# Performance work log

Hardware: AMD Instinct MI355X
Metric: run time of the kernel (lower is better)

The kernel has to match this reference:

```python
import jax, jax.numpy as jnp
import numpy as np

B, NPG, D_IN, D, L = 64, 512, 1, 128, 10
N = B * NPG
DEG = 16
E = N * DEG
EPS = 1e-5


def setup_inputs() -> dict:
    key = jax.random.key(0)
    ks = jax.random.split(key, 8)
    x = jax.random.normal(ks[0], (N, D_IN), jnp.float32)
    # edges confined within each graph: local indices + per-graph offset
    src_local = jax.random.randint(ks[1], (E,), 0, NPG)
    dst_local = jax.random.randint(ks[2], (E,), 0, NPG)
    offs = (jnp.arange(E) // (E // B)) * NPG
    edge_src = (src_local + offs).astype(jnp.int32)
    edge_dst = (dst_local + offs).astype(jnp.int32)
    batch = jnp.repeat(jnp.arange(B, dtype=jnp.int32), NPG)
    g = lambda k, s, fan: jax.random.normal(k, s, jnp.float32) / np.float32(np.sqrt(fan))
    W0 = g(ks[3], (D_IN, D), D_IN)
    b0 = jnp.zeros((D,), jnp.float32)
    W_rest = g(ks[4], (L - 1, D, D), D)
    b_rest = jnp.zeros((L - 1, D), jnp.float32)
    gamma = jnp.ones((L, D), jnp.float32)
    beta = jnp.zeros((L, D), jnp.float32)
    W_att = g(ks[5], (D, D), D)
    return dict(x=x, edge_src=edge_src, edge_dst=edge_dst, batch=batch,
                W0=W0, b0=b0, W_rest=W_rest, b_rest=b_rest,
                gamma=gamma, beta=beta, W_att=W_att)


def _gcn_conv(h, W, b, src, dst, norm_e, self_w):
    # GCNConv: h' = D^-1/2 (A + I) D^-1/2 (h W) + b  (symmetric norm, self-loops)
    h = h @ W
    msg = norm_e[:, None] * h[src]                      # [E, D] gather
    agg = jax.ops.segment_sum(msg, dst, num_segments=N)  # [N, D] scatter-add
    return agg + self_w[:, None] * h + b


def _bn_relu(h, g, b):
    mu = jnp.mean(h, axis=0)
    var = jnp.var(h, axis=0)
    return jax.nn.relu(g * (h - mu) * jax.lax.rsqrt(var + EPS) + b)


def reference(x, edge_src, edge_dst, batch, W0, b0, W_rest, b_rest, gamma, beta, W_att):
    # symmetric GCN normalization with self-loops (edge weight 1)
    deg = 1.0 + jax.ops.segment_sum(jnp.ones((E,), x.dtype), edge_dst, num_segments=N)
    dinv = jax.lax.rsqrt(deg)
    norm_e = dinv[edge_src] * dinv[edge_dst]   # [E]
    self_w = dinv * dinv                        # [N] self-loop coefficient

    h = _gcn_conv(x, W0, b0, edge_src, edge_dst, norm_e, self_w)
    h = _bn_relu(h, gamma[0], beta[0])
    for l in range(L - 1):
        h = _gcn_conv(h, W_rest[l], b_rest[l], edge_src, edge_dst, norm_e, self_w)
        h = _bn_relu(h, gamma[l + 1], beta[l + 1])

    # graph attention pooling
    mean = jax.ops.segment_sum(h, batch, num_segments=B) / jnp.float32(NPG)  # [B, D]
    tg = jnp.tanh(mean @ W_att)                                              # [B, D]
    coefs = jax.nn.sigmoid(jnp.sum(h * tg[batch], axis=1) * 10.0)            # [N]
    graph_feat = jax.ops.segment_sum(coefs[:, None] * h, batch, num_segments=B)  # [B, D]

    # to_dense_batch (equal-sized graphs -> exact reshape) + concat broadcast graph feat
    node_dense = h.reshape(B, NPG, D)
    gf = jnp.broadcast_to(graph_feat[:, None, :], (B, NPG, D))
    return jnp.concatenate([node_dense, gf], axis=-1)  # [B, NPG, 2D]
```

## Files before the change

kernel.cpp:

```cpp
#include <hip/hip_runtime.h>
#include <hip/hip_bf16.h>
#include <math.h>

#define NN 32768
#define BG 64
#define NPGC 512
#define DD 128
#define EE 524288
#define LL 10
#define EPSF 1e-5f
#define PADK 72
#define PADW 136

typedef __attribute__((ext_vector_type(8))) short short8;
typedef __attribute__((ext_vector_type(4))) float float4v;

static __device__ __forceinline__ unsigned short f2bf(float x) {
    __hip_bfloat16 b = __float2bfloat16(x);
    return *reinterpret_cast<unsigned short*>(&b);
}
static __device__ __forceinline__ float bf2f(unsigned short u) {
    unsigned int v = ((unsigned int)u) << 16;
    return __uint_as_float(v);
}
static __device__ __forceinline__ void splitbf(float x, unsigned short& h, unsigned short& l) {
    unsigned short hh = f2bf(x);
    h = hh;
    l = f2bf(x - bf2f(hh));
}


__global__ void k_histM(const int* __restrict__ src, const int* __restrict__ dst,
                        unsigned int* __restrict__ Mp, int* __restrict__ cnt) {
    int e = blockIdx.x * 256 + threadIdx.x;
    int d = dst[e], s = src[e] & 511;
    int cell = (d << 9) + s;
    atomicAdd(&Mp[cell >> 1], 1u << ((cell & 1) << 4));
    atomicAdd(&cnt[d], 1);
}

__global__ void k_dinv(const int* __restrict__ cnt, float* __restrict__ dinv) {
    int n = blockIdx.x * 256 + threadIdx.x;
    dinv[n] = rsqrtf(1.0f + (float)cnt[n]);
}

__global__ void k_conv(const unsigned int* __restrict__ Mp, unsigned short* __restrict__ Mh) {
    int idx = (blockIdx.x * 256 + threadIdx.x) * 8;
    uint4 v = *(const uint4*)(Mp + (idx >> 1));
    unsigned int c[8] = {v.x & 0xffffu, v.x >> 16, v.y & 0xffffu, v.y >> 16,
                         v.z & 0xffffu, v.z >> 16, v.w & 0xffffu, v.w >> 16};
    int diag = (idx >> 9) & 511;
    int cb = idx & 511;
    unsigned short us[8];
    #pragma unroll
    for (int j = 0; j < 8; j++)
        us[j] = f2bf((float)(c[j] + ((cb + j == diag) ? 1u : 0u)));
    *(uint4*)(Mh + idx) = *(uint4*)us;
}

__global__ void k_wt(const float* __restrict__ Wr, unsigned short* __restrict__ Wt_h,
                     unsigned short* __restrict__ Wt_l) {
    int idx = blockIdx.x * 256 + threadIdx.x;
    int l = idx >> 14, rem = idx & 16383;
    int fp = rem >> 7, f = rem & 127;
    unsigned short h, lo;
    splitbf(Wr[l * 16384 + f * 128 + fp], h, lo);
    Wt_h[idx] = h;
    Wt_l[idx] = lo;
}

__global__ void k_l0(const float* __restrict__ x, const float* __restrict__ W0,
                     const float* __restrict__ dinv,
                     unsigned short* __restrict__ hwT_h, unsigned short* __restrict__ hwT_l) {
    int u = blockIdx.x * 256 + threadIdx.x;
    int f = u >> 12, n0 = (u & 4095) * 8;
    float w = W0[f];
    float4 xa = *(const float4*)(x + n0);
    float4 xb = *(const float4*)(x + n0 + 4);
    float4 da = *(const float4*)(dinv + n0);
    float4 db = *(const float4*)(dinv + n0 + 4);
    float v[8] = {xa.x * w * da.x, xa.y * w * da.y, xa.z * w * da.z, xa.w * w * da.w,
                  xb.x * w * db.x, xb.y * w * db.y, xb.z * w * db.z, xb.w * w * db.w};
    unsigned short uh[8], ul[8];
    #pragma unroll
    for (int i = 0; i < 8; i++) splitbf(v[i], uh[i], ul[i]);
    *(uint4*)(hwT_h + (size_t)f * NN + n0) = *(uint4*)uh;
    *(uint4*)(hwT_l + (size_t)f * NN + n0) = *(uint4*)ul;
}

__global__ __launch_bounds__(256) void k_aggmm(const unsigned short* __restrict__ Mh,
        const unsigned short* __restrict__ hwT_h, const unsigned short* __restrict__ hwT_l,
        const float* __restrict__ dinv, const float* __restrict__ bias,
        float* __restrict__ pre, float* __restrict__ stats) {
    __shared__ unsigned short As[64 * PADK];
    __shared__ unsigned short Bs_h[128 * PADK], Bs_l[128 * PADK];
    int t = threadIdx.x, lane = t & 63, wv = t >> 6;
    int l15 = lane & 15, quad = lane >> 4;
    int b = blockIdx.x, r = b & 7, q = b >> 3;
    int g = r + 8 * (q & 7);
    int mb = (q >> 3) * 64;
    size_t arow = ((size_t)g * 512 + mb) * 512;
    size_t gcol = (size_t)g * 512;
    float4v acc[8];
    #pragma unroll
    for (int i = 0; i < 8; i++) acc[i] = (float4v)0.f;

    for (int kc = 0; kc < 512; kc += 64) {
        __syncthreads();
        {
            int i = t >> 7;
            #pragma unroll
            for (int it = 0; it < 2; it++) {
                int u = t + it * 256;
                int row = u >> 3, ko = (u & 7) * 8;
                *(uint4*)(&As[row * PADK + ko]) =
                    *(const uint4*)(Mh + arow + (size_t)row * 512 + kc + ko);
            }
            (void)i;
        }
        #pragma unroll
        for (int i = 0; i < 4; i++) {
            int u = t + i * 256;
            int f = u >> 3, ko = (u & 7) * 8;
            size_t go = (size_t)f * NN + gcol + kc + ko;
            *(uint4*)(&Bs_h[f * PADK + ko]) = *(const uint4*)(hwT_h + go);
            *(uint4*)(&Bs_l[f * PADK + ko]) = *(const uint4*)(hwT_l + go);
        }
        __syncthreads();
        int f0 = wv * 32;
        #pragma unroll
        for (int ks = 0; ks < 2; ks++) {
            int kb = ks * 32 + quad * 8;
            short8 a[4];
            #pragma unroll
            for (int mt = 0; mt < 4; mt++)
                a[mt] = *(const short8*)(&As[(mt * 16 + l15) * PADK + kb]);
            #pragma unroll
            for (int nt = 0; nt < 2; nt++) {
                short8 bh = *(const short8*)(&Bs_h[(f0 + nt * 16 + l15) * PADK + kb]);
                short8 bl = *(const short8*)(&Bs_l[(f0 + nt * 16 + l15) * PADK + kb]);
                #pragma unroll
                for (int mt = 0; mt < 4; mt++) {
                    acc[mt * 2 + nt] = __builtin_amdgcn_mfma_f32_16x16x32_bf16(a[mt], bh, acc[mt * 2 + nt], 0, 0, 0);
                    acc[mt * 2 + nt] = __builtin_amdgcn_mfma_f32_16x16x32_bf16(a[mt], bl, acc[mt * 2 + nt], 0, 0, 0);
                }
            }
        }
    }
    int gbase = g * 512 + mb;
    int fA = wv * 32 + l15;
    float bf0 = bias[fA], bf1 = bias[fA + 16];
    float cs[2] = {0.f, 0.f}, cq[2] = {0.f, 0.f};
    #pragma unroll
    for (int mt = 0; mt < 4; mt++) {
        int n0 = gbase + mt * 16 + quad * 4;
        float4 dv = *(const float4*)(dinv + n0);
        #pragma unroll
        for (int nt = 0; nt < 2; nt++) {
            int f = fA + nt * 16;
            float bf = nt ? bf1 : bf0;
            float4v a = acc[mt * 2 + nt];
            float v0 = fmaf(dv.x, a[0], bf);
            float v1 = fmaf(dv.y, a[1], bf);
            float v2 = fmaf(dv.z, a[2], bf);
            float v3 = fmaf(dv.w, a[3], bf);
            pre[(size_t)(n0 + 0) * 128 + f] = v0;
            pre[(size_t)(n0 + 1) * 128 + f] = v1;
            pre[(size_t)(n0 + 2) * 128 + f] = v2;
            pre[(size_t)(n0 + 3) * 128 + f] = v3;
            cs[nt] += v0 + v1 + v2 + v3;
            cq[nt] = fmaf(v0, v0, cq[nt]); cq[nt] = fmaf(v1, v1, cq[nt]);
            cq[nt] = fmaf(v2, v2, cq[nt]); cq[nt] = fmaf(v3, v3, cq[nt]);
        }
    }
    #pragma unroll
    for (int nt = 0; nt < 2; nt++) {
        float cs_ = cs[nt], cq_ = cq[nt];
        cs_ += __shfl_xor(cs_, 16); cs_ += __shfl_xor(cs_, 32);
        cq_ += __shfl_xor(cq_, 16); cq_ += __shfl_xor(cq_, 32);
        if (quad == 0) {
            atomicAdd(&stats[fA + nt * 16], cs_);
            atomicAdd(&stats[128 + fA + nt * 16], cq_);
        }
    }
}

__global__ __launch_bounds__(256) void k_mmT(const float* __restrict__ pre,
        const float* __restrict__ stats, const float* __restrict__ gamma,
        const float* __restrict__ beta, const float* __restrict__ dinv,
        const unsigned short* __restrict__ Wt_h, const unsigned short* __restrict__ Wt_l,
        unsigned short* __restrict__ hwT_h, unsigned short* __restrict__ hwT_l) {
    __shared__ unsigned short Xs_h[64 * PADW], Xs_l[64 * PADW];
    __shared__ float scL[256];
    int t = threadIdx.x, lane = t & 63, wv = t >> 6;
    int l15 = lane & 15, quad = lane >> 4;
    int b = blockIdx.x, r = b & 7, q = b >> 3;
    int g = r + 8 * (q & 7);
    int nb = g * NPGC + (q >> 3) * 64;
    if (t < 128) {
        float mu = stats[t] * (1.0f / NN);
        float var = stats[128 + t] * (1.0f / NN) - mu * mu;
        float s = gamma[t] * rsqrtf(var + EPSF);
        scL[t] = s;
        scL[128 + t] = fmaf(-mu, s, beta[t]);
    }
    __syncthreads();
    #pragma unroll
    for (int i = 0; i < 4; i++) {
        int u = t + i * 256;
        int n = u >> 4, fo = (u & 15) * 8;
        const float* pp = pre + (size_t)(nb + n) * 128 + fo;
        float4 v0 = *(const float4*)(pp);
        float4 v1 = *(const float4*)(pp + 4);
        float4 s0 = *(const float4*)(&scL[fo]);
        float4 s1 = *(const float4*)(&scL[fo + 4]);
        float4 h0 = *(const float4*)(&scL[128 + fo]);
        float4 h1 = *(const float4*)(&scL[128 + fo + 4]);
        float v[8] = {fmaxf(fmaf(v0.x, s0.x, h0.x), 0.f),
                      fmaxf(fmaf(v0.y, s0.y, h0.y), 0.f),
                      fmaxf(fmaf(v0.z, s0.z, h0.z), 0.f),
                      fmaxf(fmaf(v0.w, s0.w, h0.w), 0.f),
                      fmaxf(fmaf(v1.x, s1.x, h1.x), 0.f),
                      fmaxf(fmaf(v1.y, s1.y, h1.y), 0.f),
                      fmaxf(fmaf(v1.z, s1.z, h1.z), 0.f),
                      fmaxf(fmaf(v1.w, s1.w, h1.w), 0.f)};
        unsigned short uh[8], ul[8];
        #pragma unroll
        for (int j = 0; j < 8; j++) splitbf(v[j], uh[j], ul[j]);
        *(uint4*)(&Xs_h[n * PADW + fo]) = *(uint4*)uh;
        *(uint4*)(&Xs_l[n * PADW + fo]) = *(uint4*)ul;
    }
    __syncthreads();
    int m0 = wv * 32;
    short8 wh[2][4], wl[2][4];
    #pragma unroll
    for (int mt = 0; mt < 2; mt++)
        #pragma unroll
        for (int kt = 0; kt < 4; kt++) {
            int ad = (m0 + mt * 16 + l15) * 128 + kt * 32 + quad * 8;
            wh[mt][kt] = *(const short8*)(Wt_h + ad);
            wl[mt][kt] = *(const short8*)(Wt_l + ad);
        }
    float4v acc[8];
    #pragma unroll
    for (int i = 0; i < 8; i++) acc[i] = (float4v)0.f;
    #pragma unroll
    for (int kt = 0; kt < 4; kt++) {
        int kb = kt * 32 + quad * 8;
        #pragma unroll
        for (int nt = 0; nt < 4; nt++) {
            short8 bh = *(const short8*)(&Xs_h[(nt * 16 + l15) * PADW + kb]);
            short8 bl = *(const short8*)(&Xs_l[(nt * 16 + l15) * PADW + kb]);
            #pragma unroll
            for (int mt = 0; mt < 2; mt++) {
                acc[mt * 4 + nt] = __builtin_amdgcn_mfma_f32_16x16x32_bf16(wh[mt][kt], bh, acc[mt * 4 + nt], 0, 0, 0);
                acc[mt * 4 + nt] = __builtin_amdgcn_mfma_f32_16x16x32_bf16(wh[mt][kt], bl, acc[mt * 4 + nt], 0, 0, 0);
                acc[mt * 4 + nt] = __builtin_amdgcn_mfma_f32_16x16x32_bf16(wl[mt][kt], bh, acc[mt * 4 + nt], 0, 0, 0);
            }
        }
    }
    #pragma unroll
    for (int mt = 0; mt < 2; mt++) {
        #pragma unroll
        for (int nt = 0; nt < 4; nt++) {
            int n = nb + nt * 16 + l15;
            float dv = dinv[n];
            int fp0 = wv * 32 + mt * 16 + quad * 4;
            float4v a = acc[mt * 4 + nt];
            #pragma unroll
            for (int rg = 0; rg < 4; rg++) {
                unsigned short h, lo;
                splitbf(dv * a[rg], h, lo);
                hwT_h[(size_t)(fp0 + rg) * NN + n] = h;
                hwT_l[(size_t)(fp0 + rg) * NN + n] = lo;
            }
        }
    }
}

__global__ __launch_bounds__(256) void k_bn_pool(float* __restrict__ pre,
        const float* __restrict__ stats, const float* __restrict__ gamma,
        const float* __restrict__ beta, float* __restrict__ meansum) {
    __shared__ float ssum[256];
    __shared__ float scL[256];
    int t = threadIdx.x;
    int b = blockIdx.x, r = b & 7, q = b >> 3;
    int g = r + 8 * (q & 7);
    int nb = g * NPGC + (q >> 3) * 64;
    if (t < 128) {
        float mu = stats[t] * (1.0f / NN);
        float var = stats[128 + t] * (1.0f / NN) - mu * mu;
        float s = gamma[t] * rsqrtf(var + EPSF);
        scL[t] = s;
        scL[128 + t] = fmaf(-mu, s, beta[t]);
    }
    __syncthreads();
    int f = t & 127;
    float s = scL[f], sh = scL[128 + f];
    float lsum = 0.f;
    int base = nb * 128;
    for (int i = 0; i < 32; i++) {
        int idx = base + i * 256 + t;
        float v = fmaxf(fmaf(pre[idx], s, sh), 0.f);
        pre[idx] = v;
        lsum += v;
    }
    ssum[t] = lsum;
    __syncthreads();
    if (t < 128) atomicAdd(&meansum[g * 128 + f], ssum[t] + ssum[t + 128]);
}

__global__ void k_tg(const float* __restrict__ meansum, const float* __restrict__ Watt,
                     float* __restrict__ tg) {
    __shared__ float m[128];
    int g = blockIdx.x, t = threadIdx.x;
    m[t] = meansum[g * 128 + t] * (1.0f / NPGC);
    __syncthreads();
    float a2 = 0.f;
    for (int k = 0; k < 128; k++) a2 = fmaf(m[k], Watt[k * 128 + t], a2);
    tg[g * 128 + t] = tanhf(a2);
}

__global__ __launch_bounds__(256) void k_coef_gf(const float* __restrict__ h,
        const float* __restrict__ tg, float* __restrict__ gf) {
    __shared__ float tgs[128];
    __shared__ float coef[64];
    int t = threadIdx.x;
    int b = blockIdx.x, r = b & 7, q = b >> 3;
    int g = r + 8 * (q & 7);
    int n0 = (q >> 3) * 64;
    if (t < 128) tgs[t] = tg[g * 128 + t];
    __syncthreads();
    int wid = t >> 6, lane = t & 63;
    const float* hp = h + (size_t)g * NPGC * 128;
    for (int j = wid; j < 64; j += 4) {
        int n = n0 + j;
        float p = hp[n * 128 + lane] * tgs[lane] + hp[n * 128 + 64 + lane] * tgs[64 + lane];
        for (int off = 32; off; off >>= 1) p += __shfl_xor(p, off);
        if (lane == 0) coef[j] = 1.0f / (1.0f + expf(-10.0f * p));
    }
    __syncthreads();
    int f = t & 127, half = t >> 7;
    float acc = 0.f;
    for (int j = 0; j < 32; j++) {
        int jj = half * 32 + j;
        acc = fmaf(coef[jj], hp[(n0 + jj) * 128 + f], acc);
    }
    atomicAdd(&gf[g * 128 + f], acc);
}

__global__ void k_out(const float* __restrict__ h, const float* __restrict__ gf,
                      float* __restrict__ out) {
    int idx = blockIdx.x * 256 + threadIdx.x;
    int c4 = (idx & 63) * 4;
    int n = idx >> 6;
    int g = n >> 9;
    float4 v = (c4 < 128) ? *(const float4*)(h + (size_t)n * 128 + c4)
                          : *(const float4*)(gf + g * 128 + (c4 - 128));
    *(float4*)(out + (size_t)idx * 4) = v;
}

extern "C" void kernel_launch(void* const* d_in, const int* in_sizes, int n_in,
                              void* d_out, int out_size, void* d_ws, size_t ws_size,
                              hipStream_t stream) {
    const float* x     = (const float*)d_in[0];
    const int*   esrc  = (const int*)d_in[1];
    const int*   edst  = (const int*)d_in[2];
    const float* W0    = (const float*)d_in[4];
    const float* b0    = (const float*)d_in[5];
    const float* Wr    = (const float*)d_in[6];
    const float* br    = (const float*)d_in[7];
    const float* gamma = (const float*)d_in[8];
    const float* beta  = (const float*)d_in[9];
    const float* Watt  = (const float*)d_in[10];
    float* out = (float*)d_out;
    float* ws  = (float*)d_ws;

    int*   cnt     = (int*)(ws + 0);
    float* dinv    = ws + 32768;
    float* stats   = ws + 65536;
    float* tgbuf   = ws + 68096;
    float* meansum = ws + 76288;
    float* gf      = ws + 84480;
    unsigned short* Wt_h  = (unsigned short*)(ws + 92672);
    unsigned short* Wt_l  = (unsigned short*)(ws + 166400);
    unsigned short* hwT_h = (unsigned short*)(ws + 240128);
    unsigned short* hwT_l = (unsigned short*)(ws + 2337280);
    unsigned short* Mh    = (unsigned short*)(ws + 4434432);
    unsigned int* Mp = (unsigned int*)(ws + 12823040);
    float* pre     = ws + 12823040;

    hipMemsetAsync(cnt, 0, NN * sizeof(int), stream);
    hipMemsetAsync(stats, 0, LL * 256 * sizeof(float), stream);
    hipMemsetAsync(meansum, 0, BG * 128 * sizeof(float), stream);
    hipMemsetAsync(gf, 0, BG * 128 * sizeof(float), stream);
    hipMemsetAsync(Mp, 0, (size_t)NN * 256 * sizeof(int), stream);

    k_histM<<<EE / 256, 256, 0, stream>>>(esrc, edst, Mp, cnt);
    k_dinv<<<NN / 256, 256, 0, stream>>>(cnt, dinv);
    k_conv<<<NN * 512 / 8 / 256, 256, 0, stream>>>(Mp, Mh);
    k_wt<<<9 * 16384 / 256, 256, 0, stream>>>(Wr, Wt_h, Wt_l);
    k_l0<<<128 * (NN / 8) / 256, 256, 0, stream>>>(x, W0, dinv, hwT_h, hwT_l);

    for (int l = 0; l < LL; l++) {
        const float* bias = (l == 0) ? b0 : br + (l - 1) * DD;
        k_aggmm<<<NN / 64, 256, 0, stream>>>(Mh, hwT_h, hwT_l, dinv, bias,
                                             pre, stats + l * 256);
        if (l < LL - 1)
            k_mmT<<<NN / 64, 256, 0, stream>>>(pre, stats + l * 256, gamma + l * DD,
                                               beta + l * DD, dinv, Wt_h + l * 16384,
                                               Wt_l + l * 16384, hwT_h, hwT_l);
        else
            k_bn_pool<<<NN / 64, 256, 0, stream>>>(pre, stats + l * 256, gamma + l * DD,
                                                   beta + l * DD, meansum);
    }
    k_tg<<<BG, 128, 0, stream>>>(meansum, Watt, tgbuf);
    k_coef_gf<<<NN / 64, 256, 0, stream>>>(pre, tgbuf, gf);
    k_out<<<NN * 64 / 256, 256, 0, stream>>>(pre, gf, out);
}
```

Measured before the change: 549.2 us.

## Enlarge aggregation tile to 128 rows with direct-to-LDS swizzled loads

The aggregation GEMM kernel now covers 128 node rows per block with 512 threads instead of 64 rows with 256, so each staged tile of bf16 hi/lo features serves twice as many rows. Tiles are copied with global_load_lds straight into shared memory, skipping the register round trip. The padded LDS layout is replaced by an XOR-style block swizzle so fragment reads stay free of bank conflicts. The cost is fewer blocks (256) and less occupancy per CU, and the kernel still has no double buffering, so global-to-LDS latency is still exposed at each barrier.

```diff
diff --git a/kernel.cpp b/kernel.cpp
--- a/kernel.cpp
+++ b/kernel.cpp
@@ -9,7 +9,6 @@
 #define EE 524288
 #define LL 10
 #define EPSF 1e-5f
-#define PADK 72
 #define PADW 136
 
 typedef __attribute__((ext_vector_type(8))) short short8;
@@ -27,6 +26,12 @@
     unsigned short hh = f2bf(x);
     h = hh;
     l = f2bf(x - bf2f(hh));
+}
+
+static __device__ __forceinline__ void load_lds16(const unsigned short* g, unsigned short* l) {
+    __builtin_amdgcn_global_load_lds(
+        (const __attribute__((address_space(1))) unsigned int*)g,
+        (__attribute__((address_space(3))) unsigned int*)l, 16, 0, 0);
 }
 
 
@@ -88,67 +93,70 @@
     *(uint4*)(hwT_l + (size_t)f * NN + n0) = *(uint4*)ul;
 }
 
-__global__ __launch_bounds__(256) void k_aggmm(const unsigned short* __restrict__ Mh,
+__global__ __launch_bounds__(512) void k_aggmm(const unsigned short* __restrict__ Mh,
         const unsigned short* __restrict__ hwT_h, const unsigned short* __restrict__ hwT_l,
         const float* __restrict__ dinv, const float* __restrict__ bias,
         float* __restrict__ pre, float* __restrict__ stats) {
-    __shared__ unsigned short As[64 * PADK];
-    __shared__ unsigned short Bs_h[128 * PADK], Bs_l[128 * PADK];
-    int t = threadIdx.x, lane = t & 63, wv = t >> 6;
+    __shared__ unsigned short As[128 * 64];
+    __shared__ unsigned short Bs_h[128 * 64], Bs_l[128 * 64];
+    int t = threadIdx.x, lane = t & 63, w = t >> 6;
     int l15 = lane & 15, quad = lane >> 4;
     int b = blockIdx.x, r = b & 7, q = b >> 3;
     int g = r + 8 * (q & 7);
-    int mb = (q >> 3) * 64;
+    int mb = (q >> 3) * 128;
     size_t arow = ((size_t)g * 512 + mb) * 512;
     size_t gcol = (size_t)g * 512;
+    int dh = w >> 2;
+    int f0 = (w & 3) * 32;
+    int srow0 = w * 16;
+    int lrow = lane >> 3;
+    int lblk = lane & 7;
     float4v acc[8];
     #pragma unroll
     for (int i = 0; i < 8; i++) acc[i] = (float4v)0.f;
 
     for (int kc = 0; kc < 512; kc += 64) {
         __syncthreads();
-        {
-            int i = t >> 7;
-            #pragma unroll
-            for (int it = 0; it < 2; it++) {
-                int u = t + it * 256;
-                int row = u >> 3, ko = (u & 7) * 8;
-                *(uint4*)(&As[row * PADK + ko]) =
-                    *(const uint4*)(Mh + arow + (size_t)row * 512 + kc + ko);
-            }
-            (void)i;
-        }
-        #pragma unroll
-        for (int i = 0; i < 4; i++) {
-            int u = t + i * 256;
-            int f = u >> 3, ko = (u & 7) * 8;
-            size_t go = (size_t)f * NN + gcol + kc + ko;
-            *(uint4*)(&Bs_h[f * PADK + ko]) = *(const uint4*)(hwT_h + go);
-            *(uint4*)(&Bs_l[f * PADK + ko]) = *(const uint4*)(hwT_l + go);
+        #pragma unroll
+        for (int it = 0; it < 2; it++) {
+            int row = srow0 + it * 8 + lrow;
+            int bl = (lblk - row) & 7;
+            int go = kc + bl * 8;
+            unsigned short* lb;
+            lb = &As[(srow0 + it * 8) * 64];
+            load_lds16(Mh + arow + (size_t)row * 512 + go, lb);
+            size_t gb = (size_t)row * NN + gcol + go;
+            lb = &Bs_h[(srow0 + it * 8) * 64];
+            load_lds16(hwT_h + gb, lb);
+            lb = &Bs_l[(srow0 + it * 8) * 64];
+            load_lds16(hwT_l + gb, lb);
         }
         __syncthreads();
-        int f0 = wv * 32;
         #pragma unroll
         for (int ks = 0; ks < 2; ks++) {
-            int kb = ks * 32 + quad * 8;
+            int bl0 = ks * 4 + quad;
             short8 a[4];
             #pragma unroll
-            for (int mt = 0; mt < 4; mt++)
-                a[mt] = *(const short8*)(&As[(mt * 16 + l15) * PADK + kb]);
+            for (int mt = 0; mt < 4; mt++) {
+                int m = dh * 64 + mt * 16 + l15;
+                a[mt] = *(const short8*)(&As[m * 64 + ((bl0 + m) & 7) * 8]);
+            }
             #pragma unroll
             for (int nt = 0; nt < 2; nt++) {
-                short8 bh = *(const short8*)(&Bs_h[(f0 + nt * 16 + l15) * PADK + kb]);
-                short8 bl = *(const short8*)(&Bs_l[(f0 + nt * 16 + l15) * PADK + kb]);
+                int f = f0 + nt * 16 + l15;
+                int p = f * 64 + ((bl0 + f) & 7) * 8;
+                short8 bh = *(const short8*)(&Bs_h[p]);
+                short8 blo = *(const short8*)(&Bs_l[p]);
                 #pragma unroll
                 for (int mt = 0; mt < 4; mt++) {
                     acc[mt * 2 + nt] = __builtin_amdgcn_mfma_f32_16x16x32_bf16(a[mt], bh, acc[mt * 2 + nt], 0, 0, 0);
-                    acc[mt * 2 + nt] = __builtin_amdgcn_mfma_f32_16x16x32_bf16(a[mt], bl, acc[mt * 2 + nt], 0, 0, 0);
+                    acc[mt * 2 + nt] = __builtin_amdgcn_mfma_f32_16x16x32_bf16(a[mt], blo, acc[mt * 2 + nt], 0, 0, 0);
                 }
             }
         }
     }
-    int gbase = g * 512 + mb;
-    int fA = wv * 32 + l15;
+    int gbase = g * 512 + mb + dh * 64;
+    int fA = f0 + l15;
     float bf0 = bias[fA], bf1 = bias[fA + 16];
     float cs[2] = {0.f, 0.f}, cq[2] = {0.f, 0.f};
     #pragma unroll
@@ -404,8 +412,8 @@
 
     for (int l = 0; l < LL; l++) {
         const float* bias = (l == 0) ? b0 : br + (l - 1) * DD;
-        k_aggmm<<<NN / 64, 256, 0, stream>>>(Mh, hwT_h, hwT_l, dinv, bias,
-                                             pre, stats + l * 256);
+        k_aggmm<<<NN / 128, 512, 0, stream>>>(Mh, hwT_h, hwT_l, dinv, bias,
+                                              pre, stats + l * 256);
         if (l < LL - 1)
             k_mmT<<<NN / 64, 256, 0, stream>>>(pre, stats + l * 256, gamma + l * DD,
                                                beta + l * DD, dinv, Wt_h + l * 16384,
```

After: 564.1 us. 1.03x slower.

## Enlarge aggregation GEMM row tile, register-prefetch next K chunk, fuse tg into coef kernel

Applied to the files above, without the earlier changes.

The dense per-graph aggregation GEMM now computes 128 rows per block instead of 64, so each loaded tile of node features is reused across twice as many adjacency rows, and the grid halves. The next K chunk of global data is prefetched into registers while MFMAs run on the current LDS tile, which overlaps load latency with compute. The small tanh(mean@W_att) kernel is folded into the coefficient/pooling kernel; each block recomputes its graph's 128-wide vector, saving one launch at the cost of redundant work. The larger tile doubles accumulator and prefetch register use and raises LDS, which may reduce occupancy, and the grid of 256 blocks may underfill the GPU.

```diff
diff --git a/kernel.cpp b/kernel.cpp
--- a/kernel.cpp
+++ b/kernel.cpp
@@ -92,55 +92,65 @@
         const unsigned short* __restrict__ hwT_h, const unsigned short* __restrict__ hwT_l,
         const float* __restrict__ dinv, const float* __restrict__ bias,
         float* __restrict__ pre, float* __restrict__ stats) {
-    __shared__ unsigned short As[64 * PADK];
+    __shared__ unsigned short As[128 * PADK];
     __shared__ unsigned short Bs_h[128 * PADK], Bs_l[128 * PADK];
     int t = threadIdx.x, lane = t & 63, wv = t >> 6;
     int l15 = lane & 15, quad = lane >> 4;
     int b = blockIdx.x, r = b & 7, q = b >> 3;
     int g = r + 8 * (q & 7);
-    int mb = (q >> 3) * 64;
+    int mb = (q >> 3) * 128;
     size_t arow = ((size_t)g * 512 + mb) * 512;
     size_t gcol = (size_t)g * 512;
-    float4v acc[8];
-    #pragma unroll
-    for (int i = 0; i < 8; i++) acc[i] = (float4v)0.f;
-
-    for (int kc = 0; kc < 512; kc += 64) {
+    float4v acc[16];
+    #pragma unroll
+    for (int i = 0; i < 16; i++) acc[i] = (float4v)0.f;
+
+    uint4 pa[4], pbh[4], pbl[4];
+    #pragma unroll
+    for (int i = 0; i < 4; i++) {
+        int u = t + i * 256;
+        int row = u >> 3, ko = (u & 7) * 8;
+        pa[i]  = *(const uint4*)(Mh + arow + (size_t)row * 512 + ko);
+        pbh[i] = *(const uint4*)(hwT_h + (size_t)row * NN + gcol + ko);
+        pbl[i] = *(const uint4*)(hwT_l + (size_t)row * NN + gcol + ko);
+    }
+
+    for (int c = 0; c < 8; c++) {
         __syncthreads();
-        {
-            int i = t >> 7;
-            #pragma unroll
-            for (int it = 0; it < 2; it++) {
-                int u = t + it * 256;
-                int row = u >> 3, ko = (u & 7) * 8;
-                *(uint4*)(&As[row * PADK + ko]) =
-                    *(const uint4*)(Mh + arow + (size_t)row * 512 + kc + ko);
-            }
-            (void)i;
-        }
         #pragma unroll
         for (int i = 0; i < 4; i++) {
             int u = t + i * 256;
-            int f = u >> 3, ko = (u & 7) * 8;
-            size_t go = (size_t)f * NN + gcol + kc + ko;
-            *(uint4*)(&Bs_h[f * PADK + ko]) = *(const uint4*)(hwT_h + go);
-            *(uint4*)(&Bs_l[f * PADK + ko]) = *(const uint4*)(hwT_l + go);
+            int row = u >> 3, ko = (u & 7) * 8;
+            *(uint4*)(&As[row * PADK + ko]) = pa[i];
+            *(uint4*)(&Bs_h[row * PADK + ko]) = pbh[i];
+            *(uint4*)(&Bs_l[row * PADK + ko]) = pbl[i];
         }
         __syncthreads();
+        if (c < 7) {
+            int kc = (c + 1) * 64;
+            #pragma unroll
+            for (int i = 0; i < 4; i++) {
+                int u = t + i * 256;
+                int row = u >> 3, ko = (u & 7) * 8;
+                pa[i]  = *(const uint4*)(Mh + arow + (size_t)row * 512 + kc + ko);
+                pbh[i] = *(const uint4*)(hwT_h + (size_t)row * NN + gcol + kc + ko);
+                pbl[i] = *(const uint4*)(hwT_l + (size_t)row * NN + gcol + kc + ko);
+            }
+        }
         int f0 = wv * 32;
         #pragma unroll
         for (int ks = 0; ks < 2; ks++) {
             int kb = ks * 32 + quad * 8;
-            short8 a[4];
+            short8 a[8];
             #pragma unroll
-            for (int mt = 0; mt < 4; mt++)
+            for (int mt = 0; mt < 8; mt++)
                 a[mt] = *(const short8*)(&As[(mt * 16 + l15) * PADK + kb]);
             #pragma unroll
             for (int nt = 0; nt < 2; nt++) {
                 short8 bh = *(const short8*)(&Bs_h[(f0 + nt * 16 + l15) * PADK + kb]);
                 short8 bl = *(const short8*)(&Bs_l[(f0 + nt * 16 + l15) * PADK + kb]);
                 #pragma unroll
-                for (int mt = 0; mt < 4; mt++) {
+                for (int mt = 0; mt < 8; mt++) {
                     acc[mt * 2 + nt] = __builtin_amdgcn_mfma_f32_16x16x32_bf16(a[mt], bh, acc[mt * 2 + nt], 0, 0, 0);
                     acc[mt * 2 + nt] = __builtin_amdgcn_mfma_f32_16x16x32_bf16(a[mt], bl, acc[mt * 2 + nt], 0, 0, 0);
                 }
@@ -152,7 +162,7 @@
     float bf0 = bias[fA], bf1 = bias[fA + 16];
     float cs[2] = {0.f, 0.f}, cq[2] = {0.f, 0.f};
     #pragma unroll
-    for (int mt = 0; mt < 4; mt++) {
+    for (int mt = 0; mt < 8; mt++) {
         int n0 = gbase + mt * 16 + quad * 4;
         float4 dv = *(const float4*)(dinv + n0);
         #pragma unroll
@@ -310,26 +320,23 @@
     if (t < 128) atomicAdd(&meansum[g * 128 + f], ssum[t] + ssum[t + 128]);
 }
 
-__global__ void k_tg(const float* __restrict__ meansum, const float* __restrict__ Watt,
-                     float* __restrict__ tg) {
+__global__ __launch_bounds__(256) void k_coef_gf(const float* __restrict__ h,
+        const float* __restrict__ meansum, const float* __restrict__ Watt,
+        float* __restrict__ gf) {
     __shared__ float m[128];
-    int g = blockIdx.x, t = threadIdx.x;
-    m[t] = meansum[g * 128 + t] * (1.0f / NPGC);
-    __syncthreads();
-    float a2 = 0.f;
-    for (int k = 0; k < 128; k++) a2 = fmaf(m[k], Watt[k * 128 + t], a2);
-    tg[g * 128 + t] = tanhf(a2);
-}
-
-__global__ __launch_bounds__(256) void k_coef_gf(const float* __restrict__ h,
-        const float* __restrict__ tg, float* __restrict__ gf) {
     __shared__ float tgs[128];
     __shared__ float coef[64];
     int t = threadIdx.x;
     int b = blockIdx.x, r = b & 7, q = b >> 3;
     int g = r + 8 * (q & 7);
     int n0 = (q >> 3) * 64;
-    if (t < 128) tgs[t] = tg[g * 128 + t];
+    if (t < 128) m[t] = meansum[g * 128 + t] * (1.0f / NPGC);
+    __syncthreads();
+    if (t < 128) {
+        float a2 = 0.f;
+        for (int k = 0; k < 128; k++) a2 = fmaf(m[k], Watt[k * 128 + t], a2);
+        tgs[t] = tanhf(a2);
+    }
     __syncthreads();
     int wid = t >> 6, lane = t & 63;
     const float* hp = h + (size_t)g * NPGC * 128;
@@ -379,7 +386,6 @@
     int*   cnt     = (int*)(ws + 0);
     float* dinv    = ws + 32768;
     float* stats   = ws + 65536;
-    float* tgbuf   = ws + 68096;
     float* meansum = ws + 76288;
     float* gf      = ws + 84480;
     unsigned short* Wt_h  = (unsigned short*)(ws + 92672);
@@ -404,8 +410,8 @@
 
     for (int l = 0; l < LL; l++) {
         const float* bias = (l == 0) ? b0 : br + (l - 1) * DD;
-        k_aggmm<<<NN / 64, 256, 0, stream>>>(Mh, hwT_h, hwT_l, dinv, bias,
-                                             pre, stats + l * 256);
+        k_aggmm<<<NN / 128, 256, 0, stream>>>(Mh, hwT_h, hwT_l, dinv, bias,
+                                              pre, stats + l * 256);
         if (l < LL - 1)
             k_mmT<<<NN / 64, 256, 0, stream>>>(pre, stats + l * 256, gamma + l * DD,
                                                beta + l * DD, dinv, Wt_h + l * 16384,
@@ -414,7 +420,6 @@
             k_bn_pool<<<NN / 64, 256, 0, stream>>>(pre, stats + l * 256, gamma + l * DD,
                                                    beta + l * DD, meansum);
     }
-    k_tg<<<BG, 128, 0, stream>>>(meansum, Watt, tgbuf);
-    k_coef_gf<<<NN / 64, 256, 0, stream>>>(pre, tgbuf, gf);
+    k_coef_gf<<<NN / 64, 256, 0, stream>>>(pre, meansum, Watt, gf);
     k_out<<<NN * 64 / 256, 256, 0, stream>>>(pre, gf, out);
 }
```

Measured after the change: 856.3 us. +55.9%, slower.
